# Optimization experiments

Measured on AMD Instinct MI355X. Metric: run time of the kernel, lower is better.

The kernel has to match this reference:

```python
import jax, jax.numpy as jnp
import numpy as np

B, T, F = 16, 16384, 32
C = 64          # residual_channels == skip_channels
L = 10          # num_layers
K = 3           # kernel_size
OUT = 1
DILATIONS = [2 ** (i % 10) for i in range(L)]


def causal_conv1d(x, w, b, dilation):
    # x: [B,C_in,T], w: [C_out,C_in,K] -> [B,C_out,T], left-padded (causal)
    pad = (w.shape[-1] - 1) * dilation
    y = jax.lax.conv_general_dilated(
        x, w, window_strides=(1,), padding=[(pad, 0)],
        rhs_dilation=(dilation,), dimension_numbers=('NCT', 'OIT', 'NCT'))
    return y + b[None, :, None]


def conv1x1(x, w, b):
    # x: [B,C_in,T], w: [C_out,C_in] -> [B,C_out,T]
    return jnp.einsum('oi,bit->bot', w, x) + b[None, :, None]


def setup_inputs() -> dict:
    key = jax.random.key(0)
    ks = jax.random.split(key, 16)
    s = 0.1
    inp = {
        'x': jax.random.normal(ks[0], (B, T, F), jnp.float32),
        'w_in': jax.random.normal(ks[1], (C, F, 1), jnp.float32) * s,
        'b_in': jnp.zeros((C,), jnp.float32),
        'fw': jax.random.normal(ks[2], (L, C, C, K), jnp.float32) * s,
        'fb': jnp.zeros((L, C), jnp.float32),
        'gw': jax.random.normal(ks[3], (L, C, C, K), jnp.float32) * s,
        'gb': jnp.zeros((L, C), jnp.float32),
        'rw': jax.random.normal(ks[4], (L, C, C), jnp.float32) * s,
        'rb': jnp.zeros((L, C), jnp.float32),
        'sw': jax.random.normal(ks[5], (L, C, C), jnp.float32) * s,
        'sb': jnp.zeros((L, C), jnp.float32),
        'ow1': jax.random.normal(ks[6], (C, C), jnp.float32) * s,
        'ob1': jnp.zeros((C,), jnp.float32),
        'ow2': jax.random.normal(ks[7], (OUT, C), jnp.float32) * s,
        'ob2': jnp.zeros((OUT,), jnp.float32),
    }
    return inp


def reference(x, w_in, b_in, fw, fb, gw, gb, rw, rb, sw, sb, ow1, ob1, ow2, ob2):
    h = jnp.transpose(x, (0, 2, 1))                 # [B,F,T]
    h = causal_conv1d(h, w_in, b_in, 1)             # [B,C,T] (1x1 causal input conv)
    skip_sum = jnp.zeros_like(h[:, :C, :]) * 0.0
    skip_sum = jnp.zeros((h.shape[0], C, h.shape[2]), h.dtype)
    for i, d in enumerate(DILATIONS):
        filt = jnp.tanh(causal_conv1d(h, fw[i], fb[i], d))
        gate = jax.nn.sigmoid(causal_conv1d(h, gw[i], gb[i], d))
        act = filt * gate
        residual = conv1x1(act, rw[i], rb[i])
        skip = conv1x1(act, sw[i], sb[i])
        h = (h + residual) * 0.7071
        skip_sum = skip_sum + skip
    out = jax.nn.relu(skip_sum)
    out = jax.nn.relu(conv1x1(out, ow1, ob1))
    out = conv1x1(out, ow2, ob2)                    # [B,OUT,T]
    return jnp.transpose(out, (0, 2, 1))            # [B,T,OUT]
```

## Files before the change

kernel.cpp:

```cpp
#include <hip/hip_runtime.h>
#include <math.h>

#define Bn 16
#define Tn 16384
#define Fn 32
#define Cn 64
#define Ln 10
#define ST 76

typedef _Float16 v8h  __attribute__((ext_vector_type(8)));
typedef _Float16 v4h  __attribute__((ext_vector_type(4)));
typedef float    v16f __attribute__((ext_vector_type(16)));
typedef float    v4f  __attribute__((ext_vector_type(4)));

__global__ __launch_bounds__(256) void k_prep(const float* __restrict__ fw,
                                              const float* __restrict__ gw,
                                              const float* __restrict__ rw,
                                              const float* __restrict__ sw,
                                              _Float16* __restrict__ wfgP,
                                              _Float16* __restrict__ rsP)
{
    int gid = blockIdx.x * 256 + threadIdx.x;
    if (gid < Ln * 24576) {
        int l      = gid / 24576;
        int rem    = gid % 24576;
        int chunk  = rem >> 9;
        int within = rem & 511;
        int lane   = within >> 3, j = within & 7;
        int ch32 = chunk & 1;
        int fg   = (chunk >> 1) & 1;
        int kc   = (chunk >> 2) & 3;
        int tap  = chunk >> 4;
        int co = ch32 * 32 + (lane & 31);
        int ci = kc * 16 + (lane >> 5) * 8 + j;
        const float* wsrc = fg ? gw : fw;
        wfgP[gid] = (_Float16)wsrc[((l * 64 + co) * 64 + ci) * 3 + tap];
    }
    int gid2 = gid - Ln * 24576;
    if (gid2 >= 0 && gid2 < Ln * 8192) {
        int l      = gid2 / 8192;
        int rem    = gid2 % 8192;
        int chunk  = rem >> 9;
        int within = rem & 511;
        int lane   = within >> 3, j = within & 7;
        int ch32 = chunk & 1;
        int rsi  = (chunk >> 1) & 1;
        int kc   = chunk >> 2;
        int co = ch32 * 32 + (lane & 31);
        int ci = kc * 16 + (lane >> 5) * 8 + j;
        const float* wsrc = rsi ? sw : rw;
        rsP[gid2] = (_Float16)wsrc[(l * 64 + co) * 64 + ci];
    }
}

__device__ __forceinline__ int xcd_swizzle(int bx, int nblk)
{
    return (bx & 7) * (nblk >> 3) + (bx >> 3);
}

__global__ __launch_bounds__(256) void k_input(const float* __restrict__ x,
                                               const float* __restrict__ w_in,
                                               const float* __restrict__ b_in,
                                               _Float16* __restrict__ h)
{
    __shared__ _Float16 HT[256 * 64];
    const int tid = threadIdx.x;
    const int blk = xcd_swizzle(blockIdx.x, Tn / 256);
    const int t0  = blk * 256;
    const int t   = t0 + tid;
    const int bb  = blockIdx.y;
    const float* xp = x + ((size_t)bb * Tn + t) * Fn;
    float xv[32];
    #pragma unroll
    for (int i = 0; i < 8; ++i) {
        v4f v = *(const v4f*)&xp[i * 4];
        xv[i*4+0] = v[0]; xv[i*4+1] = v[1]; xv[i*4+2] = v[2]; xv[i*4+3] = v[3];
    }
    #pragma unroll
    for (int c8 = 0; c8 < 8; ++c8) {
        v8h o;
        #pragma unroll
        for (int j = 0; j < 8; ++j) {
            int c = c8 * 8 + j;
            float a = b_in[c];
            #pragma unroll
            for (int f = 0; f < 32; ++f) a = fmaf(w_in[c * 32 + f], xv[f], a);
            o[j] = (_Float16)a;
        }
        const int p = (c8 + tid) & 7;
        *(v8h*)&HT[tid * 64 + p * 8] = o;
    }
    __syncthreads();
    _Float16* hp = h + ((size_t)bb * Tn + t0) * 64;
    #pragma unroll
    for (int it = 0; it < 8; ++it) {
        const int g  = it * 256 + tid;
        const int tl = g >> 3, c8 = g & 7;
        const int p  = (c8 + tl) & 7;
        *(v8h*)&hp[g * 8] = *(const v8h*)&HT[tl * 64 + p * 8];
    }
}

__global__ __launch_bounds__(256, 4) void k_layer_u(
    const _Float16* __restrict__ hin, _Float16* __restrict__ hout,
    _Float16* __restrict__ skip,
    const _Float16* __restrict__ wfg,
    const _Float16* __restrict__ rs,
    const float* __restrict__ fb, const float* __restrict__ gb,
    const float* __restrict__ rb, const float* __restrict__ sb,
    const int dil, const float skip_scale)
{
    __shared__ _Float16 UB[128 * ST];

    const int tid  = threadIdx.x;
    const int lane = tid & 63;
    const int wv   = tid >> 6;
    const int ch32 = wv & 1;
    const int ch   = ch32 * 32;
    const int tw   = (wv >> 1) * 32;
    const int hl   = lane >> 5;
    const int ln31 = lane & 31;
    const int bb   = blockIdx.y;
    const int t0   = xcd_swizzle(blockIdx.x, Tn / 64) * 64;
    const size_t hbase = (size_t)bb * Tn * 64;

    v8h zero8;
    #pragma unroll
    for (int j = 0; j < 8; ++j) zero8[j] = (_Float16)0.f;

    const int s_tl = tid >> 3;
    const int s_c  = (tid & 7) * 8;

#define WOFF(TAP, KC, FG) (((((TAP) * 4 + (KC)) * 2 + (FG)) * 2 + ch32) * 512 + lane * 8)
#define RSOFF(KC, RSI)    ((((KC) * 2 + (RSI)) * 2 + ch32) * 512 + lane * 8)

    #pragma unroll
    for (int it = 0; it < 4; ++it) {
        int row = s_tl + it * 32;
        int tg  = t0 - 64 + row;
        v8h v = zero8;
        if (tg >= 0) v = *(const v8h*)&hin[hbase + (size_t)tg * 64 + s_c];
        *(v8h*)&UB[row * ST + s_c] = v;
    }

    v16f accF, accG;
    #pragma unroll
    for (int q = 0; q < 4; ++q) {
        v4f fv = *(const v4f*)&fb[ch + 8 * q + 4 * hl];
        v4f gv = *(const v4f*)&gb[ch + 8 * q + 4 * hl];
        #pragma unroll
        for (int r = 0; r < 4; ++r) {
            accF[q * 4 + r] = fv[r];
            accG[q * 4 + r] = gv[r];
        }
    }
    __syncthreads();

    #pragma unroll
    for (int tap = 0; tap < 3; ++tap) {
        const int rbase = 64 + tw - (2 - tap) * dil;
        #pragma unroll
        for (int kc = 0; kc < 4; ++kc) {
            const int kof = kc * 16 + hl * 8;
            v8h aF = *(const v8h*)&wfg[WOFF(tap, kc, 0)];
            v8h aG = *(const v8h*)&wfg[WOFF(tap, kc, 1)];
            v8h b0 = *(const v8h*)&UB[(rbase + ln31) * ST + kof];
            accF = __builtin_amdgcn_mfma_f32_32x32x16_f16(aF, b0, accF, 0, 0, 0);
            accG = __builtin_amdgcn_mfma_f32_32x32x16_f16(aG, b0, accG, 0, 0, 0);
        }
    }
    __syncthreads();

    #pragma unroll
    for (int q = 0; q < 4; ++q) {
        v4h av;
        #pragma unroll
        for (int r = 0; r < 4; ++r) {
            float f = accF[q * 4 + r];
            float g = accG[q * 4 + r];
            float A = __expf(2.f * f);
            float B = __expf(-g);
            float tA = A + 1.f;
            float den = fmaf(tA, B, tA);
            av[r] = (_Float16)((A - 1.f) * __builtin_amdgcn_rcpf(den));
        }
        *(v4h*)&UB[(tw + ln31) * ST + ch + 8 * q + 4 * hl] = av;
    }
    __syncthreads();

    v16f accR, accS;
    #pragma unroll
    for (int q = 0; q < 4; ++q) {
        v4f rv = *(const v4f*)&rb[ch + 8 * q + 4 * hl];
        v4f sv = *(const v4f*)&sb[ch + 8 * q + 4 * hl];
        #pragma unroll
        for (int r = 0; r < 4; ++r) {
            accR[q * 4 + r] = rv[r];
            accS[q * 4 + r] = sv[r];
        }
    }
    #pragma unroll
    for (int kc = 0; kc < 4; ++kc) {
        const int kof = kc * 16 + hl * 8;
        v8h aR = *(const v8h*)&rs[RSOFF(kc, 0)];
        v8h aS = *(const v8h*)&rs[RSOFF(kc, 1)];
        v8h b0 = *(const v8h*)&UB[(tw + ln31) * ST + kof];
        accR = __builtin_amdgcn_mfma_f32_32x32x16_f16(aR, b0, accR, 0, 0, 0);
        accS = __builtin_amdgcn_mfma_f32_32x32x16_f16(aS, b0, accS, 0, 0, 0);
    }

    #pragma unroll
    for (int q = 0; q < 4; ++q) {
        _Float16* cell = &UB[(64 + tw + ln31) * ST + ch + 8 * q + 4 * hl];
        v4h hv = *(const v4h*)cell;
        v4h hn;
        #pragma unroll
        for (int r = 0; r < 4; ++r)
            hn[r] = (_Float16)(((float)hv[r] + accR[q * 4 + r]) * 0.7071f);
        *(v4h*)cell = hn;
    }
    __syncthreads();

    #pragma unroll
    for (int q = 0; q < 4; ++q) {
        v4h sn;
        #pragma unroll
        for (int r = 0; r < 4; ++r)
            sn[r] = (_Float16)accS[q * 4 + r];
        *(v4h*)&UB[(tw + ln31) * ST + ch + 8 * q + 4 * hl] = sn;
    }
    __syncthreads();

    #pragma unroll
    for (int it = 0; it < 2; ++it) {
        int tl = s_tl + it * 32;
        *(v8h*)&hout[hbase + (size_t)(t0 + tl) * 64 + s_c] =
            *(const v8h*)&UB[(64 + tl) * ST + s_c];
    }
    #pragma unroll
    for (int it = 0; it < 2; ++it) {
        int tl = s_tl + it * 32;
        const size_t base = hbase + (size_t)(t0 + tl) * 64 + s_c;
        v8h sk = *(const v8h*)&skip[base];
        v8h pv = *(const v8h*)&UB[tl * ST + s_c];
        v8h sn;
        #pragma unroll
        for (int r = 0; r < 8; ++r)
            sn[r] = (_Float16)((float)sk[r] * skip_scale + (float)pv[r]);
        *(v8h*)&skip[base] = sn;
    }
#undef WOFF
#undef RSOFF
}

__global__ __launch_bounds__(256, 4) void k_layer(
    const _Float16* __restrict__ hin, _Float16* __restrict__ hout,
    _Float16* __restrict__ skip,
    const _Float16* __restrict__ wfg,
    const _Float16* __restrict__ rs,
    const float* __restrict__ fb, const float* __restrict__ gb,
    const float* __restrict__ rb, const float* __restrict__ sb,
    const int dil, const float skip_scale)
{
    __shared__ _Float16 P0[64 * ST];
    __shared__ _Float16 P1[64 * ST];

    const int tid  = threadIdx.x;
    const int lane = tid & 63;
    const int wv   = tid >> 6;
    const int ch32 = wv & 1;
    const int ch   = ch32 * 32;
    const int tw   = (wv >> 1) * 32;
    const int hl   = lane >> 5;
    const int ln31 = lane & 31;
    const int bb   = blockIdx.y;
    const int t0   = xcd_swizzle(blockIdx.x, Tn / 64) * 64;
    const size_t hbase = (size_t)bb * Tn * 64;

    v8h zero8;
    #pragma unroll
    for (int j = 0; j < 8; ++j) zero8[j] = (_Float16)0.f;

    const int s_tl = tid >> 3;
    const int s_c  = (tid & 7) * 8;

#define STAGE(DST, OFF) do {                                                  \
    _Pragma("unroll")                                                         \
    for (int it = 0; it < 2; ++it) {                                          \
        int tl = s_tl + it * 32;                                              \
        int tg = t0 + tl - (OFF);                                             \
        v8h v = zero8;                                                        \
        if (tg >= 0) v = *(const v8h*)&hin[hbase + (size_t)tg * 64 + s_c];    \
        *(v8h*)&(DST)[tl * ST + s_c] = v;                                     \
    } } while (0)

#define WOFF(TAP, KC, FG) (((((TAP) * 4 + (KC)) * 2 + (FG)) * 2 + ch32) * 512 + lane * 8)
#define RSOFF(KC, RSI)    ((((KC) * 2 + (RSI)) * 2 + ch32) * 512 + lane * 8)

#define MFMA_TAP(SRC, TAP) do {                                               \
    _Pragma("unroll")                                                         \
    for (int kc = 0; kc < 4; ++kc) {                                          \
        const int kof = kc * 16 + hl * 8;                                     \
        v8h aF = *(const v8h*)&wfg[WOFF(TAP, kc, 0)];                         \
        v8h aG = *(const v8h*)&wfg[WOFF(TAP, kc, 1)];                         \
        v8h b0 = *(const v8h*)&(SRC)[(tw + ln31) * ST + kof];                 \
        accF = __builtin_amdgcn_mfma_f32_32x32x16_f16(aF, b0, accF, 0, 0, 0); \
        accG = __builtin_amdgcn_mfma_f32_32x32x16_f16(aG, b0, accG, 0, 0, 0); \
    } } while (0)

    v16f accF, accG;
    #pragma unroll
    for (int q = 0; q < 4; ++q) {
        v4f fv = *(const v4f*)&fb[ch + 8 * q + 4 * hl];
        v4f gv = *(const v4f*)&gb[ch + 8 * q + 4 * hl];
        #pragma unroll
        for (int r = 0; r < 4; ++r) {
            accF[q * 4 + r] = fv[r];
            accG[q * 4 + r] = gv[r];
        }
    }

    STAGE(P0, 2 * dil);
    __syncthreads();
    STAGE(P1, dil);
    MFMA_TAP(P0, 0);
    __syncthreads();
    STAGE(P0, 0);
    MFMA_TAP(P1, 1);
    __syncthreads();
    MFMA_TAP(P0, 2);

    #pragma unroll
    for (int q = 0; q < 4; ++q) {
        v4h av;
        #pragma unroll
        for (int r = 0; r < 4; ++r) {
            float f = accF[q * 4 + r];
            float g = accG[q * 4 + r];
            float A = __expf(2.f * f);
            float B = __expf(-g);
            float tA = A + 1.f;
            float den = fmaf(tA, B, tA);
            av[r] = (_Float16)((A - 1.f) * __builtin_amdgcn_rcpf(den));
        }
        *(v4h*)&P1[(tw + ln31) * ST + ch + 8 * q + 4 * hl] = av;
    }
    __syncthreads();

    v16f accR, accS;
    #pragma unroll
    for (int q = 0; q < 4; ++q) {
        v4f rv = *(const v4f*)&rb[ch + 8 * q + 4 * hl];
        v4f sv = *(const v4f*)&sb[ch + 8 * q + 4 * hl];
        #pragma unroll
        for (int r = 0; r < 4; ++r) {
            accR[q * 4 + r] = rv[r];
            accS[q * 4 + r] = sv[r];
        }
    }

    #pragma unroll
    for (int kc = 0; kc < 4; ++kc) {
        const int kof = kc * 16 + hl * 8;
        v8h aR = *(const v8h*)&rs[RSOFF(kc, 0)];
        v8h aS = *(const v8h*)&rs[RSOFF(kc, 1)];
        v8h b0 = *(const v8h*)&P1[(tw + ln31) * ST + kof];
        accR = __builtin_amdgcn_mfma_f32_32x32x16_f16(aR, b0, accR, 0, 0, 0);
        accS = __builtin_amdgcn_mfma_f32_32x32x16_f16(aS, b0, accS, 0, 0, 0);
    }

    #pragma unroll
    for (int q = 0; q < 4; ++q) {
        _Float16* cell = &P0[(tw + ln31) * ST + ch + 8 * q + 4 * hl];
        v4h hv = *(const v4h*)cell;
        v4h hn;
        #pragma unroll
        for (int r = 0; r < 4; ++r)
            hn[r] = (_Float16)(((float)hv[r] + accR[q * 4 + r]) * 0.7071f);
        *(v4h*)cell = hn;
    }
    __syncthreads();

    #pragma unroll
    for (int q = 0; q < 4; ++q) {
        v4h sn;
        #pragma unroll
        for (int r = 0; r < 4; ++r)
            sn[r] = (_Float16)accS[q * 4 + r];
        *(v4h*)&P1[(tw + ln31) * ST + ch + 8 * q + 4 * hl] = sn;
    }
    #pragma unroll
    for (int it = 0; it < 2; ++it) {
        int tl = s_tl + it * 32;
        *(v8h*)&hout[hbase + (size_t)(t0 + tl) * 64 + s_c] = *(const v8h*)&P0[tl * ST + s_c];
    }
    __syncthreads();

    #pragma unroll
    for (int it = 0; it < 2; ++it) {
        int tl = s_tl + it * 32;
        const size_t base = hbase + (size_t)(t0 + tl) * 64 + s_c;
        v8h sk = *(const v8h*)&skip[base];
        v8h pv = *(const v8h*)&P1[tl * ST + s_c];
        v8h sn;
        #pragma unroll
        for (int r = 0; r < 8; ++r)
            sn[r] = (_Float16)((float)sk[r] * skip_scale + (float)pv[r]);
        *(v8h*)&skip[base] = sn;
    }
#undef STAGE
#undef MFMA_TAP
#undef WOFF
#undef RSOFF
}

__global__ __launch_bounds__(256) void k_out(const _Float16* __restrict__ skip,
                                             const float* __restrict__ ow1,
                                             const float* __restrict__ ob1,
                                             const float* __restrict__ ow2,
                                             const float* __restrict__ ob2,
                                             float* __restrict__ out)
{
    const int blk = xcd_swizzle(blockIdx.x, Tn / 256);
    const int t  = blk * 256 + threadIdx.x;
    const int bb = blockIdx.y;
    const _Float16* sp = skip + ((size_t)bb * Tn + t) * 64;
    float y[64];
    #pragma unroll
    for (int i = 0; i < 8; ++i) {
        v8h v = *(const v8h*)&sp[i * 8];
        #pragma unroll
        for (int j = 0; j < 8; ++j) y[i * 8 + j] = fmaxf((float)v[j], 0.f);
    }
    float o = ob2[0];
    for (int co = 0; co < 64; ++co) {
        float a0 = ob1[co], a1 = 0.f;
        #pragma unroll
        for (int ci = 0; ci < 64; ci += 2) {
            a0 = fmaf(ow1[co * 64 + ci],     y[ci],     a0);
            a1 = fmaf(ow1[co * 64 + ci + 1], y[ci + 1], a1);
        }
        o = fmaf(ow2[co], fmaxf(a0 + a1, 0.f), o);
    }
    out[(size_t)bb * Tn + t] = o;
}

extern "C" void kernel_launch(void* const* d_in, const int* in_sizes, int n_in,
                              void* d_out, int out_size, void* d_ws, size_t ws_size,
                              hipStream_t stream)
{
    const float* x    = (const float*)d_in[0];
    const float* w_in = (const float*)d_in[1];
    const float* b_in = (const float*)d_in[2];
    const float* fw   = (const float*)d_in[3];
    const float* fb   = (const float*)d_in[4];
    const float* gw   = (const float*)d_in[5];
    const float* gb   = (const float*)d_in[6];
    const float* rw   = (const float*)d_in[7];
    const float* rb   = (const float*)d_in[8];
    const float* sw   = (const float*)d_in[9];
    const float* sb   = (const float*)d_in[10];
    const float* ow1  = (const float*)d_in[11];
    const float* ob1  = (const float*)d_in[12];
    const float* ow2  = (const float*)d_in[13];
    const float* ob2  = (const float*)d_in[14];
    float* out = (float*)d_out;

    const size_t n = (size_t)Bn * Tn * 64;
    _Float16* hA    = (_Float16*)d_ws;
    _Float16* hB    = hA + n;
    _Float16* skip  = hB + n;
    _Float16* wfg16 = skip + n;
    _Float16* rs16  = wfg16 + (size_t)Ln * 24576;

    dim3 blk(256);
    k_prep<<<dim3((Ln * 24576 + Ln * 8192 + 255) / 256), blk, 0, stream>>>(
        fw, gw, rw, sw, wfg16, rs16);
    k_input<<<dim3(Tn / 256, Bn), blk, 0, stream>>>(x, w_in, b_in, hA);

    const _Float16* cur = hA;
    _Float16* nxt = hB;
    for (int l = 0; l < Ln; ++l) {
        const int d = 1 << l;
        if (d <= 32) {
            k_layer_u<<<dim3(Tn / 64, Bn), blk, 0, stream>>>(
                cur, nxt, skip,
                wfg16 + (size_t)l * 24576, rs16 + (size_t)l * 8192,
                fb + l * Cn, gb + l * Cn, rb + l * Cn, sb + l * Cn,
                d, (l == 0) ? 0.f : 1.f);
        } else {
            k_layer<<<dim3(Tn / 64, Bn), blk, 0, stream>>>(
                cur, nxt, skip,
                wfg16 + (size_t)l * 24576, rs16 + (size_t)l * 8192,
                fb + l * Cn, gb + l * Cn, rb + l * Cn, sb + l * Cn,
                d, 1.f);
        }
        const _Float16* tmp = nxt; nxt = (_Float16*)cur; cur = tmp;
    }

    k_out<<<dim3(Tn / 256, Bn), blk, 0, stream>>>(skip, ow1, ob1, ow2, ob2, out);
}
```

Measured before the change: 534.7 us.

## Fuse consecutive small-dilation WaveNet layers into one pair kernel

Layers 0-5 now run as three kernels, each computing two consecutive layers per tile. The first layer is evaluated over an extra 64-step halo so the second layer's dilated taps can read the intermediate h from shared memory, which avoids a global write and read of h and a skip read-modify-write between the two layers. The last layer skips computing and writing h since nothing reads it, and layer 0 no longer reads the uninitialized skip buffer. The cost is redundant halo compute, more shared memory, and launch bounds lowered from 4 to 3 blocks per CU.

```diff
diff --git a/kernel.cpp b/kernel.cpp
--- a/kernel.cpp
+++ b/kernel.cpp
@@ -101,16 +101,19 @@
     }
 }
 
-__global__ __launch_bounds__(256, 4) void k_layer_u(
+__global__ __launch_bounds__(256, 3) void k_pair(
     const _Float16* __restrict__ hin, _Float16* __restrict__ hout,
     _Float16* __restrict__ skip,
-    const _Float16* __restrict__ wfg,
-    const _Float16* __restrict__ rs,
-    const float* __restrict__ fb, const float* __restrict__ gb,
-    const float* __restrict__ rb, const float* __restrict__ sb,
+    const _Float16* __restrict__ wfgA, const _Float16* __restrict__ rsA,
+    const _Float16* __restrict__ wfgB, const _Float16* __restrict__ rsB,
+    const float* __restrict__ fbA, const float* __restrict__ gbA,
+    const float* __restrict__ rbA, const float* __restrict__ sbA,
+    const float* __restrict__ fbB, const float* __restrict__ gbB,
+    const float* __restrict__ rbB, const float* __restrict__ sbB,
     const int dil, const float skip_scale)
 {
-    __shared__ _Float16 UB[128 * ST];
+    __shared__ _Float16 UB[160 * ST];
+    __shared__ _Float16 HB[128 * ST];
 
     const int tid  = threadIdx.x;
     const int lane = tid & 63;
@@ -135,119 +138,194 @@
 #define RSOFF(KC, RSI)    ((((KC) * 2 + (RSI)) * 2 + ch32) * 512 + lane * 8)
 
     #pragma unroll
-    for (int it = 0; it < 4; ++it) {
+    for (int it = 0; it < 5; ++it) {
         int row = s_tl + it * 32;
-        int tg  = t0 - 64 + row;
+        int tg  = t0 - 96 + row;
         v8h v = zero8;
         if (tg >= 0) v = *(const v8h*)&hin[hbase + (size_t)tg * 64 + s_c];
         *(v8h*)&UB[row * ST + s_c] = v;
     }
-
-    v16f accF, accG;
-    #pragma unroll
-    for (int q = 0; q < 4; ++q) {
-        v4f fv = *(const v4f*)&fb[ch + 8 * q + 4 * hl];
-        v4f gv = *(const v4f*)&gb[ch + 8 * q + 4 * hl];
-        #pragma unroll
-        for (int r = 0; r < 4; ++r) {
-            accF[q * 4 + r] = fv[r];
-            accG[q * 4 + r] = gv[r];
-        }
-    }
-    __syncthreads();
-
-    #pragma unroll
-    for (int tap = 0; tap < 3; ++tap) {
-        const int rbase = 64 + tw - (2 - tap) * dil;
+    __syncthreads();
+
+    v16f accSl;
+
+    #pragma unroll
+    for (int c = 0; c < 2; ++c) {
+        const int mrow = c * 64 + tw + ln31;
+        v16f accF, accG;
+        #pragma unroll
+        for (int q = 0; q < 4; ++q) {
+            v4f fv = *(const v4f*)&fbA[ch + 8 * q + 4 * hl];
+            v4f gv = *(const v4f*)&gbA[ch + 8 * q + 4 * hl];
+            #pragma unroll
+            for (int r = 0; r < 4; ++r) { accF[q*4+r] = fv[r]; accG[q*4+r] = gv[r]; }
+        }
+        #pragma unroll
+        for (int tap = 0; tap < 3; ++tap) {
+            const int ur = 32 + c * 64 + tw - (2 - tap) * dil;
+            #pragma unroll
+            for (int kc = 0; kc < 4; ++kc) {
+                const int kof = kc * 16 + hl * 8;
+                v8h aF = *(const v8h*)&wfgA[WOFF(tap, kc, 0)];
+                v8h aG = *(const v8h*)&wfgA[WOFF(tap, kc, 1)];
+                v8h b0 = *(const v8h*)&UB[(ur + ln31) * ST + kof];
+                accF = __builtin_amdgcn_mfma_f32_32x32x16_f16(aF, b0, accF, 0, 0, 0);
+                accG = __builtin_amdgcn_mfma_f32_32x32x16_f16(aG, b0, accG, 0, 0, 0);
+            }
+        }
+        #pragma unroll
+        for (int q = 0; q < 4; ++q) {
+            v4h av;
+            #pragma unroll
+            for (int r = 0; r < 4; ++r) {
+                float f = accF[q * 4 + r];
+                float g = accG[q * 4 + r];
+                float A = __expf(2.f * f);
+                float B = __expf(-g);
+                float tA = A + 1.f;
+                float den = fmaf(tA, B, tA);
+                av[r] = (_Float16)((A - 1.f) * __builtin_amdgcn_rcpf(den));
+            }
+            *(v4h*)&HB[mrow * ST + ch + 8 * q + 4 * hl] = av;
+        }
+        __syncthreads();
+
+        v16f accR, accS;
+        #pragma unroll
+        for (int q = 0; q < 4; ++q) {
+            v4f rv = *(const v4f*)&rbA[ch + 8 * q + 4 * hl];
+            v4f sv = *(const v4f*)&sbA[ch + 8 * q + 4 * hl];
+            #pragma unroll
+            for (int r = 0; r < 4; ++r) { accR[q*4+r] = rv[r]; accS[q*4+r] = sv[r]; }
+        }
         #pragma unroll
         for (int kc = 0; kc < 4; ++kc) {
             const int kof = kc * 16 + hl * 8;
-            v8h aF = *(const v8h*)&wfg[WOFF(tap, kc, 0)];
-            v8h aG = *(const v8h*)&wfg[WOFF(tap, kc, 1)];
-            v8h b0 = *(const v8h*)&UB[(rbase + ln31) * ST + kof];
-            accF = __builtin_amdgcn_mfma_f32_32x32x16_f16(aF, b0, accF, 0, 0, 0);
-            accG = __builtin_amdgcn_mfma_f32_32x32x16_f16(aG, b0, accG, 0, 0, 0);
-        }
-    }
-    __syncthreads();
-
-    #pragma unroll
-    for (int q = 0; q < 4; ++q) {
-        v4h av;
-        #pragma unroll
-        for (int r = 0; r < 4; ++r) {
-            float f = accF[q * 4 + r];
-            float g = accG[q * 4 + r];
-            float A = __expf(2.f * f);
-            float B = __expf(-g);
-            float tA = A + 1.f;
-            float den = fmaf(tA, B, tA);
-            av[r] = (_Float16)((A - 1.f) * __builtin_amdgcn_rcpf(den));
-        }
-        *(v4h*)&UB[(tw + ln31) * ST + ch + 8 * q + 4 * hl] = av;
-    }
-    __syncthreads();
-
-    v16f accR, accS;
-    #pragma unroll
-    for (int q = 0; q < 4; ++q) {
-        v4f rv = *(const v4f*)&rb[ch + 8 * q + 4 * hl];
-        v4f sv = *(const v4f*)&sb[ch + 8 * q + 4 * hl];
-        #pragma unroll
-        for (int r = 0; r < 4; ++r) {
-            accR[q * 4 + r] = rv[r];
-            accS[q * 4 + r] = sv[r];
-        }
-    }
-    #pragma unroll
-    for (int kc = 0; kc < 4; ++kc) {
-        const int kof = kc * 16 + hl * 8;
-        v8h aR = *(const v8h*)&rs[RSOFF(kc, 0)];
-        v8h aS = *(const v8h*)&rs[RSOFF(kc, 1)];
-        v8h b0 = *(const v8h*)&UB[(tw + ln31) * ST + kof];
-        accR = __builtin_amdgcn_mfma_f32_32x32x16_f16(aR, b0, accR, 0, 0, 0);
-        accS = __builtin_amdgcn_mfma_f32_32x32x16_f16(aS, b0, accS, 0, 0, 0);
-    }
-
-    #pragma unroll
-    for (int q = 0; q < 4; ++q) {
-        _Float16* cell = &UB[(64 + tw + ln31) * ST + ch + 8 * q + 4 * hl];
-        v4h hv = *(const v4h*)cell;
-        v4h hn;
-        #pragma unroll
-        for (int r = 0; r < 4; ++r)
-            hn[r] = (_Float16)(((float)hv[r] + accR[q * 4 + r]) * 0.7071f);
-        *(v4h*)cell = hn;
-    }
-    __syncthreads();
-
-    #pragma unroll
-    for (int q = 0; q < 4; ++q) {
-        v4h sn;
-        #pragma unroll
-        for (int r = 0; r < 4; ++r)
-            sn[r] = (_Float16)accS[q * 4 + r];
-        *(v4h*)&UB[(tw + ln31) * ST + ch + 8 * q + 4 * hl] = sn;
-    }
-    __syncthreads();
-
-    #pragma unroll
-    for (int it = 0; it < 2; ++it) {
-        int tl = s_tl + it * 32;
-        *(v8h*)&hout[hbase + (size_t)(t0 + tl) * 64 + s_c] =
-            *(const v8h*)&UB[(64 + tl) * ST + s_c];
-    }
-    #pragma unroll
-    for (int it = 0; it < 2; ++it) {
-        int tl = s_tl + it * 32;
-        const size_t base = hbase + (size_t)(t0 + tl) * 64 + s_c;
-        v8h sk = *(const v8h*)&skip[base];
-        v8h pv = *(const v8h*)&UB[tl * ST + s_c];
-        v8h sn;
-        #pragma unroll
-        for (int r = 0; r < 8; ++r)
-            sn[r] = (_Float16)((float)sk[r] * skip_scale + (float)pv[r]);
-        *(v8h*)&skip[base] = sn;
+            v8h aR = *(const v8h*)&rsA[RSOFF(kc, 0)];
+            v8h b0 = *(const v8h*)&HB[mrow * ST + kof];
+            accR = __builtin_amdgcn_mfma_f32_32x32x16_f16(aR, b0, accR, 0, 0, 0);
+            if (c == 1) {
+                v8h aS = *(const v8h*)&rsA[RSOFF(kc, 1)];
+                accS = __builtin_amdgcn_mfma_f32_32x32x16_f16(aS, b0, accS, 0, 0, 0);
+            }
+        }
+        __syncthreads();
+
+        const int tglob = t0 - 64 + c * 64 + tw + ln31;
+        #pragma unroll
+        for (int q = 0; q < 4; ++q) {
+            v4h hv = *(const v4h*)&UB[(32 + c * 64 + tw + ln31) * ST + ch + 8 * q + 4 * hl];
+            v4h hn;
+            #pragma unroll
+            for (int r = 0; r < 4; ++r)
+                hn[r] = (tglob >= 0)
+                      ? (_Float16)(((float)hv[r] + accR[q * 4 + r]) * 0.7071f)
+                      : (_Float16)0.f;
+            *(v4h*)&HB[mrow * ST + ch + 8 * q + 4 * hl] = hn;
+        }
+        if (c == 1) accSl = accS;
+    }
+    __syncthreads();
+
+    {
+        v16f accF, accG;
+        #pragma unroll
+        for (int q = 0; q < 4; ++q) {
+            v4f fv = *(const v4f*)&fbB[ch + 8 * q + 4 * hl];
+            v4f gv = *(const v4f*)&gbB[ch + 8 * q + 4 * hl];
+            #pragma unroll
+            for (int r = 0; r < 4; ++r) { accF[q*4+r] = fv[r]; accG[q*4+r] = gv[r]; }
+        }
+        #pragma unroll
+        for (int tap = 0; tap < 3; ++tap) {
+            const int hr = 64 + tw - (2 - tap) * 2 * dil;
+            #pragma unroll
+            for (int kc = 0; kc < 4; ++kc) {
+                const int kof = kc * 16 + hl * 8;
+                v8h aF = *(const v8h*)&wfgB[WOFF(tap, kc, 0)];
+                v8h aG = *(const v8h*)&wfgB[WOFF(tap, kc, 1)];
+                v8h b0 = *(const v8h*)&HB[(hr + ln31) * ST + kof];
+                accF = __builtin_amdgcn_mfma_f32_32x32x16_f16(aF, b0, accF, 0, 0, 0);
+                accG = __builtin_amdgcn_mfma_f32_32x32x16_f16(aG, b0, accG, 0, 0, 0);
+            }
+        }
+        #pragma unroll
+        for (int q = 0; q < 4; ++q) {
+            v4h av;
+            #pragma unroll
+            for (int r = 0; r < 4; ++r) {
+                float f = accF[q * 4 + r];
+                float g = accG[q * 4 + r];
+                float A = __expf(2.f * f);
+                float B = __expf(-g);
+                float tA = A + 1.f;
+                float den = fmaf(tA, B, tA);
+                av[r] = (_Float16)((A - 1.f) * __builtin_amdgcn_rcpf(den));
+            }
+            *(v4h*)&UB[(tw + ln31) * ST + ch + 8 * q + 4 * hl] = av;
+        }
+        __syncthreads();
+
+        v16f accR, accS;
+        #pragma unroll
+        for (int q = 0; q < 4; ++q) {
+            v4f rv = *(const v4f*)&rbB[ch + 8 * q + 4 * hl];
+            v4f sv = *(const v4f*)&sbB[ch + 8 * q + 4 * hl];
+            #pragma unroll
+            for (int r = 0; r < 4; ++r) { accR[q*4+r] = rv[r]; accS[q*4+r] = sv[r]; }
+        }
+        #pragma unroll
+        for (int kc = 0; kc < 4; ++kc) {
+            const int kof = kc * 16 + hl * 8;
+            v8h aR = *(const v8h*)&rsB[RSOFF(kc, 0)];
+            v8h aS = *(const v8h*)&rsB[RSOFF(kc, 1)];
+            v8h b0 = *(const v8h*)&UB[(tw + ln31) * ST + kof];
+            accR = __builtin_amdgcn_mfma_f32_32x32x16_f16(aR, b0, accR, 0, 0, 0);
+            accS = __builtin_amdgcn_mfma_f32_32x32x16_f16(aS, b0, accS, 0, 0, 0);
+        }
+        #pragma unroll
+        for (int q = 0; q < 4; ++q) {
+            v4h hv = *(const v4h*)&HB[(64 + tw + ln31) * ST + ch + 8 * q + 4 * hl];
+            v4h hn;
+            #pragma unroll
+            for (int r = 0; r < 4; ++r)
+                hn[r] = (_Float16)(((float)hv[r] + accR[q * 4 + r]) * 0.7071f);
+            *(v4h*)&UB[(64 + tw + ln31) * ST + ch + 8 * q + 4 * hl] = hn;
+        }
+        __syncthreads();
+
+        #pragma unroll
+        for (int q = 0; q < 4; ++q) {
+            v4h sn;
+            #pragma unroll
+            for (int r = 0; r < 4; ++r)
+                sn[r] = (_Float16)(accS[q * 4 + r] + accSl[q * 4 + r]);
+            *(v4h*)&UB[(tw + ln31) * ST + ch + 8 * q + 4 * hl] = sn;
+        }
+        #pragma unroll
+        for (int it = 0; it < 2; ++it) {
+            int tl = s_tl + it * 32;
+            *(v8h*)&hout[hbase + (size_t)(t0 + tl) * 64 + s_c] =
+                *(const v8h*)&UB[(64 + tl) * ST + s_c];
+        }
+        __syncthreads();
+
+        #pragma unroll
+        for (int it = 0; it < 2; ++it) {
+            int tl = s_tl + it * 32;
+            const size_t base = hbase + (size_t)(t0 + tl) * 64 + s_c;
+            v8h pv = *(const v8h*)&UB[tl * ST + s_c];
+            v8h sn;
+            if (skip_scale != 0.f) {
+                v8h sk = *(const v8h*)&skip[base];
+                #pragma unroll
+                for (int r = 0; r < 8; ++r)
+                    sn[r] = (_Float16)((float)sk[r] * skip_scale + (float)pv[r]);
+            } else {
+                sn = pv;
+            }
+            *(v8h*)&skip[base] = sn;
+        }
     }
 #undef WOFF
 #undef RSOFF
@@ -256,11 +334,10 @@
 __global__ __launch_bounds__(256, 4) void k_layer(
     const _Float16* __restrict__ hin, _Float16* __restrict__ hout,
     _Float16* __restrict__ skip,
-    const _Float16* __restrict__ wfg,
-    const _Float16* __restrict__ rs,
+    const _Float16* __restrict__ wfg, const _Float16* __restrict__ rs,
     const float* __restrict__ fb, const float* __restrict__ gb,
     const float* __restrict__ rb, const float* __restrict__ sb,
-    const int dil, const float skip_scale)
+    const int dil, const int write_h)
 {
     __shared__ _Float16 P0[64 * ST];
     __shared__ _Float16 P1[64 * ST];
@@ -314,10 +391,7 @@
         v4f fv = *(const v4f*)&fb[ch + 8 * q + 4 * hl];
         v4f gv = *(const v4f*)&gb[ch + 8 * q + 4 * hl];
         #pragma unroll
-        for (int r = 0; r < 4; ++r) {
-            accF[q * 4 + r] = fv[r];
-            accG[q * 4 + r] = gv[r];
-        }
+        for (int r = 0; r < 4; ++r) { accF[q*4+r] = fv[r]; accG[q*4+r] = gv[r]; }
     }
 
     STAGE(P0, 2 * dil);
@@ -353,12 +427,8 @@
         v4f rv = *(const v4f*)&rb[ch + 8 * q + 4 * hl];
         v4f sv = *(const v4f*)&sb[ch + 8 * q + 4 * hl];
         #pragma unroll
-        for (int r = 0; r < 4; ++r) {
-            accR[q * 4 + r] = rv[r];
-            accS[q * 4 + r] = sv[r];
-        }
-    }
-
+        for (int r = 0; r < 4; ++r) { accR[q*4+r] = rv[r]; accS[q*4+r] = sv[r]; }
+    }
     #pragma unroll
     for (int kc = 0; kc < 4; ++kc) {
         const int kof = kc * 16 + hl * 8;
@@ -369,15 +439,17 @@
         accS = __builtin_amdgcn_mfma_f32_32x32x16_f16(aS, b0, accS, 0, 0, 0);
     }
 
-    #pragma unroll
-    for (int q = 0; q < 4; ++q) {
-        _Float16* cell = &P0[(tw + ln31) * ST + ch + 8 * q + 4 * hl];
-        v4h hv = *(const v4h*)cell;
-        v4h hn;
-        #pragma unroll
-        for (int r = 0; r < 4; ++r)
-            hn[r] = (_Float16)(((float)hv[r] + accR[q * 4 + r]) * 0.7071f);
-        *(v4h*)cell = hn;
+    if (write_h) {
+        #pragma unroll
+        for (int q = 0; q < 4; ++q) {
+            _Float16* cell = &P0[(tw + ln31) * ST + ch + 8 * q + 4 * hl];
+            v4h hv = *(const v4h*)cell;
+            v4h hn;
+            #pragma unroll
+            for (int r = 0; r < 4; ++r)
+                hn[r] = (_Float16)(((float)hv[r] + accR[q * 4 + r]) * 0.7071f);
+            *(v4h*)cell = hn;
+        }
     }
     __syncthreads();
 
@@ -389,10 +461,12 @@
             sn[r] = (_Float16)accS[q * 4 + r];
         *(v4h*)&P1[(tw + ln31) * ST + ch + 8 * q + 4 * hl] = sn;
     }
-    #pragma unroll
-    for (int it = 0; it < 2; ++it) {
-        int tl = s_tl + it * 32;
-        *(v8h*)&hout[hbase + (size_t)(t0 + tl) * 64 + s_c] = *(const v8h*)&P0[tl * ST + s_c];
+    if (write_h) {
+        #pragma unroll
+        for (int it = 0; it < 2; ++it) {
+            int tl = s_tl + it * 32;
+            *(v8h*)&hout[hbase + (size_t)(t0 + tl) * 64 + s_c] = *(const v8h*)&P0[tl * ST + s_c];
+        }
     }
     __syncthreads();
 
@@ -405,7 +479,7 @@
         v8h sn;
         #pragma unroll
         for (int r = 0; r < 8; ++r)
-            sn[r] = (_Float16)((float)sk[r] * skip_scale + (float)pv[r]);
+            sn[r] = (_Float16)((float)sk[r] + (float)pv[r]);
         *(v8h*)&skip[base] = sn;
     }
 #undef STAGE
@@ -480,23 +554,26 @@
 
     const _Float16* cur = hA;
     _Float16* nxt = hB;
-    for (int l = 0; l < Ln; ++l) {
+    for (int l = 0; l < 6; l += 2) {
         const int d = 1 << l;
-        if (d <= 32) {
-            k_layer_u<<<dim3(Tn / 64, Bn), blk, 0, stream>>>(
-                cur, nxt, skip,
-                wfg16 + (size_t)l * 24576, rs16 + (size_t)l * 8192,
-                fb + l * Cn, gb + l * Cn, rb + l * Cn, sb + l * Cn,
-                d, (l == 0) ? 0.f : 1.f);
-        } else {
-            k_layer<<<dim3(Tn / 64, Bn), blk, 0, stream>>>(
-                cur, nxt, skip,
-                wfg16 + (size_t)l * 24576, rs16 + (size_t)l * 8192,
-                fb + l * Cn, gb + l * Cn, rb + l * Cn, sb + l * Cn,
-                d, 1.f);
-        }
+        k_pair<<<dim3(Tn / 64, Bn), blk, 0, stream>>>(
+            cur, nxt, skip,
+            wfg16 + (size_t)l * 24576,       rs16 + (size_t)l * 8192,
+            wfg16 + (size_t)(l + 1) * 24576, rs16 + (size_t)(l + 1) * 8192,
+            fb + l * Cn, gb + l * Cn, rb + l * Cn, sb + l * Cn,
+            fb + (l + 1) * Cn, gb + (l + 1) * Cn, rb + (l + 1) * Cn, sb + (l + 1) * Cn,
+            d, (l == 0) ? 0.f : 1.f);
         const _Float16* tmp = nxt; nxt = (_Float16*)cur; cur = tmp;
     }
+    for (int l = 6; l < Ln; ++l) {
+        const int d = 1 << l;
+        k_layer<<<dim3(Tn / 64, Bn), blk, 0, stream>>>(
+            cur, nxt, skip,
+            wfg16 + (size_t)l * 24576, rs16 + (size_t)l * 8192,
+            fb + l * Cn, gb + l * Cn, rb + l * Cn, sb + l * Cn,
+            d, (l == Ln - 1) ? 0 : 1);
+        const _Float16* tmp = nxt; nxt = (_Float16*)cur; cur = tmp;
+    }
 
     k_out<<<dim3(Tn / 256, Bn), blk, 0, stream>>>(skip, ow1, ob1, ow2, ob2, out);
 }
```

New measurement: 596.8 us. 1.12x slower.
